# Kernel tuning notes

Hardware: AMD Instinct MI355X
Metric: run time of the kernel (lower is better)

The kernel has to match this reference:

```python
import jax, jax.numpy as jnp
import numpy as np

SIGMA = 2.0
Z_CUTOFF = 3


def make_gaussian_kernel(sigma=SIGMA, z=Z_CUTOFF):
    # kernel_size = 2*z*sigma + 1; bump to odd if even (float math as in torch)
    ks = 2 * z * sigma + 1
    if ks % 2 == 0:
        ks += 1
    ks = int(ks)
    r = np.arange(-(ks // 2), ks // 2 + 1, dtype=np.float32)
    xx, yy = np.meshgrid(r, r, indexing='ij')
    k = np.exp(-(xx ** 2 + yy ** 2) / (2.0 * sigma ** 2))
    k = k / k.sum()
    return jnp.asarray(k.reshape(1, 1, ks, ks))  # [O=1, I=1, kh, kw]


def setup_inputs() -> dict:
    key = jax.random.key(0)
    x = jax.random.normal(key, (32, 1, 1024, 1024), dtype=jnp.float32)
    kernel = make_gaussian_kernel()
    return {"x": x, "kernel": kernel}


def reference(x, kernel):
    ks = kernel.shape[-1]
    half = ks // 2
    h_even_in = x.shape[-2] % 2 == 0
    w_even_in = x.shape[-1] % 2 == 0
    # torch F.pad order (left, right, top, bottom) -> jnp.pad ((top,bot),(left,right))
    pad_t, pad_b = half, half + int(h_even_in)
    pad_l, pad_r = half, half + int(w_even_in)
    xp = jnp.pad(x, ((0, 0), (0, 0), (pad_t, pad_b), (pad_l, pad_r)), mode='reflect')
    # cross-correlation, valid padding (matches torch conv2d with padding=0)
    y = jax.lax.conv_general_dilated(
        xp, kernel, window_strides=(1, 1), padding='VALID',
        dimension_numbers=('NCHW', 'OIHW', 'NCHW'))
    # crop based on parity of POST-conv shape, as in the torch module
    h_cut = 2 if y.shape[-2] % 2 == 0 else 1
    w_cut = 2 if y.shape[-1] % 2 == 0 else 1
    return y[:, :, :-h_cut, :-w_cut]
```

## Files before the change

kernel.cpp:

```cpp
#include <hip/hip_runtime.h>

#define KS    13
#define HALF  6
#define TY    64
#define NITER (TY + 12)
#define NK    (NITER / 2)
#define IMG_H 1024
#define IMG_W 1024

typedef float vfloat4 __attribute__((ext_vector_type(4)));

__device__ __forceinline__ int reflect_idx(int i, int n) {
    if (i < 0) i = -i;
    if (i >= n) i = 2 * n - 2 - i;
    return i;
}

struct Ctx {
    const float* xin;
    float*       o;
    float        g[KS];
    int          t;
    int          r0;
    bool         interior;
};

__device__ __forceinline__ void nt_store4(float* p, const float4& a) {
    vfloat4 v = { a.x, a.y, a.z, a.w };
    __builtin_nontemporal_store(v, reinterpret_cast<vfloat4*>(p));
}

__device__ __forceinline__ float4 h_filter(const float* srow, const Ctx& cx) {
    float f[20];
    if (cx.interior) {
        #pragma unroll
        for (int k = 0; k < 5; ++k) {
            float4 v = *reinterpret_cast<const float4*>(srow + 4 * cx.t - 8 + 4 * k);
            f[4*k+0] = v.x; f[4*k+1] = v.y; f[4*k+2] = v.z; f[4*k+3] = v.w;
        }
    } else {
        #pragma unroll
        for (int k = 0; k < 20; ++k)
            f[k] = srow[reflect_idx(4 * cx.t - 8 + k, IMG_W)];
    }
    float4 h = make_float4(0.f, 0.f, 0.f, 0.f);
    #pragma unroll
    for (int j = 0; j < KS; ++j) {
        h.x += cx.g[j] * f[2 + j];
        h.y += cx.g[j] * f[3 + j];
        h.z += cx.g[j] * f[4 + j];
        h.w += cx.g[j] * f[5 + j];
    }
    return h;
}

template<int U>
__device__ __forceinline__ void body2(int outer, const Ctx& cx, float (*s)[IMG_W],
                                      float4 (&w)[14], float4& cur0, float4& cur1)
{
    const int k = outer * 7 + U;
    if (k >= NK) return;
    const int n0 = 2 * k;
    const int bp = (k & 1) * 2;

    *reinterpret_cast<float4*>(&s[bp + 0][4 * cx.t]) = cur0;
    *reinterpret_cast<float4*>(&s[bp + 1][4 * cx.t]) = cur1;
    if (k + 1 < NK) {
        const int ra = reflect_idx(cx.r0 + n0 - 4, IMG_H);
        const int rb = reflect_idx(cx.r0 + n0 - 3, IMG_H);
        cur0 = *reinterpret_cast<const float4*>(cx.xin + (size_t)ra * IMG_W + 4 * cx.t);
        cur1 = *reinterpret_cast<const float4*>(cx.xin + (size_t)rb * IMG_W + 4 * cx.t);
    }
    __syncthreads();

    if (n0 >= 14) {
        float4 a0 = make_float4(0.f, 0.f, 0.f, 0.f);
        float4 a1 = make_float4(0.f, 0.f, 0.f, 0.f);
        #pragma unroll
        for (int j = 0; j < KS; ++j) {
            const float4 v0 = w[(2 * U + j) % 14];
            const float4 v1 = w[(2 * U + 1 + j) % 14];
            a0.x += cx.g[j] * v0.x;  a1.x += cx.g[j] * v1.x;
            a0.y += cx.g[j] * v0.y;  a1.y += cx.g[j] * v1.y;
            a0.z += cx.g[j] * v0.z;  a1.z += cx.g[j] * v1.z;
            a0.w += cx.g[j] * v0.w;  a1.w += cx.g[j] * v1.w;
        }
        nt_store4(cx.o + (size_t)(cx.r0 + n0 - 14) * IMG_W + 4 * cx.t, a0);
        nt_store4(cx.o + (size_t)(cx.r0 + n0 - 13) * IMG_W + 4 * cx.t, a1);
    }

    w[(2 * U) % 14]     = h_filter(s[bp + 0], cx);
    w[(2 * U + 1) % 14] = h_filter(s[bp + 1], cx);
}

__global__ __launch_bounds__(256) void gauss_blur_stream(
    const float* __restrict__ x, const float* __restrict__ k2d,
    float* __restrict__ out)
{
    __shared__ float s[4][IMG_W];

    Ctx cx;
    cx.t  = threadIdx.x;
    cx.r0 = blockIdx.x * TY;
    const int img = blockIdx.y;
    cx.xin = x + (size_t)img * IMG_H * IMG_W;
    cx.o   = out + (size_t)img * IMG_H * IMG_W;
    cx.interior = (cx.t >= 2) && (cx.t <= 253);

    {
        float c   = k2d[HALF * KS + HALF];
        float inv = 1.0f / sqrtf(c);
        #pragma unroll
        for (int j = 0; j < KS; ++j) cx.g[j] = k2d[j * KS + HALF] * inv;
    }

    float4 w[14];
    float4 cur0 = *reinterpret_cast<const float4*>(
        cx.xin + (size_t)reflect_idx(cx.r0 - 6, IMG_H) * IMG_W + 4 * cx.t);
    float4 cur1 = *reinterpret_cast<const float4*>(
        cx.xin + (size_t)reflect_idx(cx.r0 - 5, IMG_H) * IMG_W + 4 * cx.t);

    for (int outer = 0; outer < 6; ++outer) {
        body2<0>(outer, cx, s, w, cur0, cur1);
        body2<1>(outer, cx, s, w, cur0, cur1);
        body2<2>(outer, cx, s, w, cur0, cur1);
        body2<3>(outer, cx, s, w, cur0, cur1);
        body2<4>(outer, cx, s, w, cur0, cur1);
        body2<5>(outer, cx, s, w, cur0, cur1);
        body2<6>(outer, cx, s, w, cur0, cur1);
    }

    {
        float4 a0 = make_float4(0.f, 0.f, 0.f, 0.f);
        float4 a1 = make_float4(0.f, 0.f, 0.f, 0.f);
        #pragma unroll
        for (int j = 0; j < KS; ++j) {
            const float4 v0 = w[(6 + j) % 14];
            const float4 v1 = w[(7 + j) % 14];
            a0.x += cx.g[j] * v0.x;  a1.x += cx.g[j] * v1.x;
            a0.y += cx.g[j] * v0.y;  a1.y += cx.g[j] * v1.y;
            a0.z += cx.g[j] * v0.z;  a1.z += cx.g[j] * v1.z;
            a0.w += cx.g[j] * v0.w;  a1.w += cx.g[j] * v1.w;
        }
        nt_store4(cx.o + (size_t)(cx.r0 + 62) * IMG_W + 4 * cx.t, a0);
        nt_store4(cx.o + (size_t)(cx.r0 + 63) * IMG_W + 4 * cx.t, a1);
    }
}

extern "C" void kernel_launch(void* const* d_in, const int* in_sizes, int n_in,
                              void* d_out, int out_size, void* d_ws, size_t ws_size,
                              hipStream_t stream) {
    const float* x   = (const float*)d_in[0];
    const float* k2d = (const float*)d_in[1];
    float*       out = (float*)d_out;

    dim3 grid(IMG_H / TY, 32);
    gauss_blur_stream<<<grid, 256, 0, stream>>>(x, k2d, out);
}
```

Measured before the change: 51.28 us.

## Split block into horizontal-filter and vertical-filter warp groups with shared staging

The block grows to 512 threads. The first 256 threads load raw rows and run the horizontal filter into a new shared buffer, while the other 256 threads read the filtered rows and run the vertical filter and stores one step behind. This is a producer/consumer pipeline meant to overlap load, horizontal and vertical work across waves. The cost is doubled LDS use, an extra shared-memory round trip and a block-wide barrier each step, and half the threads sit idle in each phase.

```diff
diff --git a/kernel.cpp b/kernel.cpp
--- a/kernel.cpp
+++ b/kernel.cpp
@@ -4,7 +4,8 @@
 #define HALF  6
 #define TY    64
 #define NITER (TY + 12)
-#define NK    (NITER / 2)
+#define NKH   38
+#define NKT   39
 #define IMG_H 1024
 #define IMG_W 1024
 
@@ -55,49 +56,65 @@
 }
 
 template<int U>
-__device__ __forceinline__ void body2(int outer, const Ctx& cx, float (*s)[IMG_W],
+__device__ __forceinline__ void body2(int outer, const Ctx& cx,
+                                      float (*sraw)[IMG_W], float (*sh)[IMG_W],
                                       float4 (&w)[14], float4& cur0, float4& cur1)
 {
     const int k = outer * 7 + U;
-    if (k >= NK) return;
-    const int n0 = 2 * k;
+    if (k >= NKT) return;
+    const bool isH = cx.t < 256;
     const int bp = (k & 1) * 2;
 
-    *reinterpret_cast<float4*>(&s[bp + 0][4 * cx.t]) = cur0;
-    *reinterpret_cast<float4*>(&s[bp + 1][4 * cx.t]) = cur1;
-    if (k + 1 < NK) {
-        const int ra = reflect_idx(cx.r0 + n0 - 4, IMG_H);
-        const int rb = reflect_idx(cx.r0 + n0 - 3, IMG_H);
-        cur0 = *reinterpret_cast<const float4*>(cx.xin + (size_t)ra * IMG_W + 4 * cx.t);
-        cur1 = *reinterpret_cast<const float4*>(cx.xin + (size_t)rb * IMG_W + 4 * cx.t);
+    if (isH && k < NKH) {
+        *reinterpret_cast<float4*>(&sraw[bp + 0][4 * cx.t]) = cur0;
+        *reinterpret_cast<float4*>(&sraw[bp + 1][4 * cx.t]) = cur1;
+        if (k + 1 < NKH) {
+            const int ra = reflect_idx(cx.r0 + 2 * k - 4, IMG_H);
+            const int rb = reflect_idx(cx.r0 + 2 * k - 3, IMG_H);
+            cur0 = *reinterpret_cast<const float4*>(cx.xin + (size_t)ra * IMG_W + 4 * cx.t);
+            cur1 = *reinterpret_cast<const float4*>(cx.xin + (size_t)rb * IMG_W + 4 * cx.t);
+        }
     }
     __syncthreads();
 
-    if (n0 >= 14) {
-        float4 a0 = make_float4(0.f, 0.f, 0.f, 0.f);
-        float4 a1 = make_float4(0.f, 0.f, 0.f, 0.f);
-        #pragma unroll
-        for (int j = 0; j < KS; ++j) {
-            const float4 v0 = w[(2 * U + j) % 14];
-            const float4 v1 = w[(2 * U + 1 + j) % 14];
-            a0.x += cx.g[j] * v0.x;  a1.x += cx.g[j] * v1.x;
-            a0.y += cx.g[j] * v0.y;  a1.y += cx.g[j] * v1.y;
-            a0.z += cx.g[j] * v0.z;  a1.z += cx.g[j] * v1.z;
-            a0.w += cx.g[j] * v0.w;  a1.w += cx.g[j] * v1.w;
+    if (isH) {
+        if (k < NKH) {
+            float4 h0 = h_filter(sraw[bp + 0], cx);
+            float4 h1 = h_filter(sraw[bp + 1], cx);
+            *reinterpret_cast<float4*>(&sh[bp + 0][4 * cx.t]) = h0;
+            *reinterpret_cast<float4*>(&sh[bp + 1][4 * cx.t]) = h1;
         }
-        nt_store4(cx.o + (size_t)(cx.r0 + n0 - 14) * IMG_W + 4 * cx.t, a0);
-        nt_store4(cx.o + (size_t)(cx.r0 + n0 - 13) * IMG_W + 4 * cx.t, a1);
+    } else {
+        const int vt = cx.t - 256;
+        const int rp = ((k - 1) & 1) * 2;
+        if (k >= 1 && k <= NKH) {
+            w[(2 * U + 12) % 14] = *reinterpret_cast<const float4*>(&sh[rp + 0][4 * vt]);
+            w[(2 * U + 13) % 14] = *reinterpret_cast<const float4*>(&sh[rp + 1][4 * vt]);
+        }
+        if (k >= 7) {
+            float4 a0 = make_float4(0.f, 0.f, 0.f, 0.f);
+            float4 a1 = make_float4(0.f, 0.f, 0.f, 0.f);
+            #pragma unroll
+            for (int j = 0; j < KS; ++j) {
+                const float4 v0 = w[(2 * U + j) % 14];
+                const float4 v1 = w[(2 * U + 1 + j) % 14];
+                a0.x += cx.g[j] * v0.x;  a1.x += cx.g[j] * v1.x;
+                a0.y += cx.g[j] * v0.y;  a1.y += cx.g[j] * v1.y;
+                a0.z += cx.g[j] * v0.z;  a1.z += cx.g[j] * v1.z;
+                a0.w += cx.g[j] * v0.w;  a1.w += cx.g[j] * v1.w;
+            }
+            nt_store4(cx.o + (size_t)(cx.r0 + 2 * k - 14) * IMG_W + 4 * vt, a0);
+            nt_store4(cx.o + (size_t)(cx.r0 + 2 * k - 13) * IMG_W + 4 * vt, a1);
+        }
     }
-
-    w[(2 * U) % 14]     = h_filter(s[bp + 0], cx);
-    w[(2 * U + 1) % 14] = h_filter(s[bp + 1], cx);
 }
 
-__global__ __launch_bounds__(256) void gauss_blur_stream(
+__global__ __launch_bounds__(512) void gauss_blur_stream(
     const float* __restrict__ x, const float* __restrict__ k2d,
     float* __restrict__ out)
 {
-    __shared__ float s[4][IMG_W];
+    __shared__ float sraw[4][IMG_W];
+    __shared__ float sh  [4][IMG_W];
 
     Ctx cx;
     cx.t  = threadIdx.x;
@@ -115,35 +132,23 @@
     }
 
     float4 w[14];
-    float4 cur0 = *reinterpret_cast<const float4*>(
-        cx.xin + (size_t)reflect_idx(cx.r0 - 6, IMG_H) * IMG_W + 4 * cx.t);
-    float4 cur1 = *reinterpret_cast<const float4*>(
-        cx.xin + (size_t)reflect_idx(cx.r0 - 5, IMG_H) * IMG_W + 4 * cx.t);
+    float4 cur0 = make_float4(0.f, 0.f, 0.f, 0.f);
+    float4 cur1 = cur0;
+    if (cx.t < 256) {
+        cur0 = *reinterpret_cast<const float4*>(
+            cx.xin + (size_t)reflect_idx(cx.r0 - 6, IMG_H) * IMG_W + 4 * cx.t);
+        cur1 = *reinterpret_cast<const float4*>(
+            cx.xin + (size_t)reflect_idx(cx.r0 - 5, IMG_H) * IMG_W + 4 * cx.t);
+    }
 
     for (int outer = 0; outer < 6; ++outer) {
-        body2<0>(outer, cx, s, w, cur0, cur1);
-        body2<1>(outer, cx, s, w, cur0, cur1);
-        body2<2>(outer, cx, s, w, cur0, cur1);
-        body2<3>(outer, cx, s, w, cur0, cur1);
-        body2<4>(outer, cx, s, w, cur0, cur1);
-        body2<5>(outer, cx, s, w, cur0, cur1);
-        body2<6>(outer, cx, s, w, cur0, cur1);
-    }
-
-    {
-        float4 a0 = make_float4(0.f, 0.f, 0.f, 0.f);
-        float4 a1 = make_float4(0.f, 0.f, 0.f, 0.f);
-        #pragma unroll
-        for (int j = 0; j < KS; ++j) {
-            const float4 v0 = w[(6 + j) % 14];
-            const float4 v1 = w[(7 + j) % 14];
-            a0.x += cx.g[j] * v0.x;  a1.x += cx.g[j] * v1.x;
-            a0.y += cx.g[j] * v0.y;  a1.y += cx.g[j] * v1.y;
-            a0.z += cx.g[j] * v0.z;  a1.z += cx.g[j] * v1.z;
-            a0.w += cx.g[j] * v0.w;  a1.w += cx.g[j] * v1.w;
-        }
-        nt_store4(cx.o + (size_t)(cx.r0 + 62) * IMG_W + 4 * cx.t, a0);
-        nt_store4(cx.o + (size_t)(cx.r0 + 63) * IMG_W + 4 * cx.t, a1);
+        body2<0>(outer, cx, sraw, sh, w, cur0, cur1);
+        body2<1>(outer, cx, sraw, sh, w, cur0, cur1);
+        body2<2>(outer, cx, sraw, sh, w, cur0, cur1);
+        body2<3>(outer, cx, sraw, sh, w, cur0, cur1);
+        body2<4>(outer, cx, sraw, sh, w, cur0, cur1);
+        body2<5>(outer, cx, sraw, sh, w, cur0, cur1);
+        body2<6>(outer, cx, sraw, sh, w, cur0, cur1);
     }
 }
 
@@ -155,5 +160,5 @@
     float*       out = (float*)d_out;
 
     dim3 grid(IMG_H / TY, 32);
-    gauss_blur_stream<<<grid, 256, 0, stream>>>(x, k2d, out);
+    gauss_blur_stream<<<grid, 512, 0, stream>>>(x, k2d, out);
 }
```

New measurement: 54.90 us. +7.1%, slower.
